# Kernel tuning notes

Measured on AMD Instinct MI355X. Metric: run time of the kernel, lower is better.

Reference implementation:

```python
import jax, jax.numpy as jnp
import numpy as np

N_NODES = 50000
N_EDGES = 800000
NODE_DIM = 32
EDGE_DIM = 16
HIDDEN = 64


def setup_inputs() -> dict:
    key = jax.random.key(0)
    ks = jax.random.split(key, 7)
    h = jax.random.normal(ks[0], (N_NODES, HIDDEN), dtype=jnp.float32)
    nf = jax.random.normal(ks[1], (N_NODES, NODE_DIM), dtype=jnp.float32)
    ef = jax.random.normal(ks[2], (N_EDGES, EDGE_DIM), dtype=jnp.float32)
    src = jax.random.randint(ks[3], (N_EDGES,), 0, N_NODES, dtype=jnp.int32)
    dst = jax.random.randint(ks[4], (N_EDGES,), 0, N_NODES, dtype=jnp.int32)
    # torch Linear weights: [out_features, in_features]
    in1 = HIDDEN + 2 * NODE_DIM + EDGE_DIM  # 144
    W1 = jax.random.normal(ks[5], (HIDDEN, in1), dtype=jnp.float32) * (1.0 / np.sqrt(in1))
    W2 = jax.random.normal(ks[6], (HIDDEN, HIDDEN), dtype=jnp.float32) * (1.0 / np.sqrt(HIDDEN))
    return {"h": h, "nf": nf, "ef": ef, "src": src, "dst": dst, "W1": W1, "W2": W2}


def reference(h, nf, ef, src, dst, W1, W2):
    n = nf.shape[0]
    # per-edge message: concat(dst.x, edge.x, src.h)  -> [E, node+edge+hidden]
    m_e = jnp.concatenate([nf[dst], ef, h[src]], axis=-1)
    # mailbox sum per destination node
    m = jax.ops.segment_sum(m_e, dst, num_segments=n)  # [N, node+edge+hidden]
    z = jnp.concatenate([nf, m], axis=-1)              # [N, hidden+2*node+edge]
    new_h = jax.nn.relu(z @ W1.T) @ W2.T               # [N, hidden]
    # DGL update_all only updates nodes that received at least one message
    deg = jax.ops.segment_sum(jnp.ones_like(dst, dtype=jnp.float32), dst, num_segments=n)
    return jnp.where(deg[:, None] > 0, new_h, h)
```

## Files before the change

### kernel.cpp

```cpp
#include <hip/hip_runtime.h>

#define NDIM 32
#define EDIM 16
#define NHID 64
#define NIN1 144
#define SCHUNK 1024
#define SPT 4

__global__ __launch_bounds__(256) void sse_hist(
    const int* __restrict__ dst, int* __restrict__ counts,
    int* __restrict__ rank,
    const float* __restrict__ W1, float* __restrict__ W1T,
    const float* __restrict__ W2, float* __restrict__ W2T, int E) {
  int e = blockIdx.x * 256 + threadIdx.x;
  if (e < NHID * NIN1) {
    int r = e / NIN1, k = e - r * NIN1;
    W1T[k * NHID + r] = W1[e];
  } else if (e < NHID * NIN1 + NHID * NHID) {
    int i = e - NHID * NIN1;
    int r = i >> 6, k = i & 63;
    W2T[k * NHID + r] = W2[i];
  }
  if (e < E) rank[e] = atomicAdd(&counts[dst[e]], 1);
}

__global__ __launch_bounds__(256) void sse_scan_part(
    const int* __restrict__ counts, int* __restrict__ bsum, int N) {
  __shared__ int ws[4];
  int t = threadIdx.x;
  int base = blockIdx.x * SCHUNK + t * SPT;
  int s = 0;
#pragma unroll
  for (int i = 0; i < SPT; ++i) {
    int idx = base + i;
    if (idx < N) s += counts[idx];
  }
  int v = s;
#pragma unroll
  for (int off = 1; off < 64; off <<= 1) v += __shfl_xor(v, off, 64);
  if ((t & 63) == 0) ws[t >> 6] = v;
  __syncthreads();
  if (t == 0) bsum[blockIdx.x] = ws[0] + ws[1] + ws[2] + ws[3];
}

__global__ __launch_bounds__(256) void sse_scan_final(
    const int* __restrict__ counts, const int* __restrict__ bsum,
    int* __restrict__ starts, int N, int nb) {
  __shared__ int ws[4];
  int t = threadIdx.x;
  int lane = t & 63, w = t >> 6;
  int boff = 0;
  for (int j = 0; j < (int)blockIdx.x; ++j) boff += bsum[j];
  int base = blockIdx.x * SCHUNK + t * SPT;
  int c[SPT];
  int s = 0;
#pragma unroll
  for (int i = 0; i < SPT; ++i) {
    int idx = base + i;
    c[i] = (idx < N) ? counts[idx] : 0;
    s += c[i];
  }
  int incl = s;
#pragma unroll
  for (int off = 1; off < 64; off <<= 1) {
    int u = __shfl_up(incl, off, 64);
    if (lane >= off) incl += u;
  }
  if (lane == 63) ws[w] = incl;
  __syncthreads();
  int woff = 0;
#pragma unroll
  for (int j = 0; j < 4; ++j)
    if (j < w) woff += ws[j];
  int run = boff + woff + (incl - s);
#pragma unroll
  for (int i = 0; i < SPT; ++i) {
    int idx = base + i;
    if (idx < N) {
      starts[idx] = run;
      run += c[i];
    }
  }
  if ((int)blockIdx.x == nb - 1 && t == 0)
    starts[N] = boff + ws[0] + ws[1] + ws[2] + ws[3];
}

__global__ __launch_bounds__(256) void sse_build(
    const int* __restrict__ src, const int* __restrict__ dst,
    const int* __restrict__ rank, const int* __restrict__ starts,
    int2* __restrict__ sedge, int E) {
  int e = blockIdx.x * 256 + threadIdx.x;
  if (e >= E) return;
  int d = dst[e];
  int pos = starts[d] + rank[e];
  sedge[pos] = make_int2(src[e], e);
}

__global__ __launch_bounds__(256) void sse_gather(
    const float* __restrict__ h, const float* __restrict__ ef,
    const int* __restrict__ starts, const int2* __restrict__ sedge,
    float* __restrict__ efsum, float* __restrict__ hsum, int N) {
  int node = blockIdx.x * 4 + (threadIdx.x >> 6);
  int lane = threadIdx.x & 63;
  if (node >= N) return;
  int st = starts[node], en = starts[node + 1];
  const float4* h4 = (const float4*)h;
  const float4* ef4 = (const float4*)ef;

  int q = lane >> 4, m = lane & 15;
  float4 ha = make_float4(0.f, 0.f, 0.f, 0.f);
  int j = st;
  for (; j + 7 < en; j += 8) {
    int s0 = sedge[j + q].x;
    int s1 = sedge[j + 4 + q].x;
    float4 v0 = h4[(size_t)s0 * 16 + m];
    float4 v1 = h4[(size_t)s1 * 16 + m];
    ha.x += v0.x + v1.x;
    ha.y += v0.y + v1.y;
    ha.z += v0.z + v1.z;
    ha.w += v0.w + v1.w;
  }
  if (j + 3 < en) {
    int s0 = sedge[j + q].x;
    float4 v0 = h4[(size_t)s0 * 16 + m];
    ha.x += v0.x; ha.y += v0.y; ha.z += v0.z; ha.w += v0.w;
    j += 4;
  }
  if (j + q < en) {
    int s0 = sedge[j + q].x;
    float4 v0 = h4[(size_t)s0 * 16 + m];
    ha.x += v0.x; ha.y += v0.y; ha.z += v0.z; ha.w += v0.w;
  }
#pragma unroll
  for (int off = 16; off < 64; off <<= 1) {
    ha.x += __shfl_xor(ha.x, off, 64);
    ha.y += __shfl_xor(ha.y, off, 64);
    ha.z += __shfl_xor(ha.z, off, 64);
    ha.w += __shfl_xor(ha.w, off, 64);
  }
  if (lane < 16) ((float4*)hsum)[(size_t)node * 16 + m] = ha;

  int eq = lane >> 2, em = lane & 3;
  float4 ea = make_float4(0.f, 0.f, 0.f, 0.f);
  for (j = st; j + 15 < en; j += 16) {
    int eid = sedge[j + eq].y;
    float4 v = ef4[(size_t)eid * 4 + em];
    ea.x += v.x; ea.y += v.y; ea.z += v.z; ea.w += v.w;
  }
  if (j + eq < en) {
    int eid = sedge[j + eq].y;
    float4 v = ef4[(size_t)eid * 4 + em];
    ea.x += v.x; ea.y += v.y; ea.z += v.z; ea.w += v.w;
  }
#pragma unroll
  for (int off = 4; off < 64; off <<= 1) {
    ea.x += __shfl_xor(ea.x, off, 64);
    ea.y += __shfl_xor(ea.y, off, 64);
    ea.z += __shfl_xor(ea.z, off, 64);
    ea.w += __shfl_xor(ea.w, off, 64);
  }
  if (lane < 4) ((float4*)efsum)[(size_t)node * 4 + em] = ea;
}

__global__ __launch_bounds__(256) void sse_node(
    const float* __restrict__ h, const float* __restrict__ nf,
    const float* __restrict__ efsum, const float* __restrict__ hsum,
    const int* __restrict__ starts, const float* __restrict__ W1T,
    const float* __restrict__ W2T, float* __restrict__ out, int N) {
  __shared__ float4 zs[36 * 64];
  __shared__ float4 as[16 * 64];

  int tid = threadIdx.x;
  int lane = tid & 63;
  int w = __builtin_amdgcn_readfirstlane(tid) >> 6;

  int node = blockIdx.x * 64 + lane;
  int nodeC = node < N ? node : N - 1;

  if (w == 0) {
    int st = starts[nodeC], en = starts[nodeC + 1];
    float dg = (float)(en - st);
    const float4* nfr = (const float4*)(nf + (size_t)nodeC * NDIM);
#pragma unroll
    for (int k4 = 0; k4 < 8; ++k4) {
      float4 v = nfr[k4];
      zs[k4 * 64 + lane] = v;
      zs[(8 + k4) * 64 + lane] =
          make_float4(dg * v.x, dg * v.y, dg * v.z, dg * v.w);
    }
  } else if (w == 1) {
    const float4* efr = (const float4*)(efsum + (size_t)nodeC * EDIM);
#pragma unroll
    for (int k4 = 0; k4 < 4; ++k4) zs[(16 + k4) * 64 + lane] = efr[k4];
  } else if (w == 2) {
    const float4* hsr = (const float4*)(hsum + (size_t)nodeC * NHID);
#pragma unroll
    for (int k4 = 0; k4 < 8; ++k4) zs[(20 + k4) * 64 + lane] = hsr[k4];
  } else {
    const float4* hsr = (const float4*)(hsum + (size_t)nodeC * NHID);
#pragma unroll
    for (int k4 = 8; k4 < 16; ++k4) zs[(20 + k4) * 64 + lane] = hsr[k4];
  }
  __syncthreads();

  const float4* w1b = (const float4*)W1T + w * 4;
  float a[16];
#pragma unroll
  for (int j = 0; j < 16; ++j) a[j] = 0.f;

#pragma unroll 2
  for (int k4 = 0; k4 < 36; ++k4) {
    float4 zv = zs[k4 * 64 + lane];
#pragma unroll
    for (int kk = 0; kk < 4; ++kk) {
      int k = k4 * 4 + kk;
      float4 w0 = w1b[k * 16 + 0];
      float4 w1 = w1b[k * 16 + 1];
      float4 w2 = w1b[k * 16 + 2];
      float4 w3 = w1b[k * 16 + 3];
      float zk = kk == 0 ? zv.x : kk == 1 ? zv.y : kk == 2 ? zv.z : zv.w;
      a[0]  = fmaf(w0.x, zk, a[0]);
      a[1]  = fmaf(w0.y, zk, a[1]);
      a[2]  = fmaf(w0.z, zk, a[2]);
      a[3]  = fmaf(w0.w, zk, a[3]);
      a[4]  = fmaf(w1.x, zk, a[4]);
      a[5]  = fmaf(w1.y, zk, a[5]);
      a[6]  = fmaf(w1.z, zk, a[6]);
      a[7]  = fmaf(w1.w, zk, a[7]);
      a[8]  = fmaf(w2.x, zk, a[8]);
      a[9]  = fmaf(w2.y, zk, a[9]);
      a[10] = fmaf(w2.z, zk, a[10]);
      a[11] = fmaf(w2.w, zk, a[11]);
      a[12] = fmaf(w3.x, zk, a[12]);
      a[13] = fmaf(w3.y, zk, a[13]);
      a[14] = fmaf(w3.z, zk, a[14]);
      a[15] = fmaf(w3.w, zk, a[15]);
    }
  }

#pragma unroll
  for (int j4 = 0; j4 < 4; ++j4)
    as[(w * 4 + j4) * 64 + lane] =
        make_float4(fmaxf(a[j4 * 4 + 0], 0.f), fmaxf(a[j4 * 4 + 1], 0.f),
                    fmaxf(a[j4 * 4 + 2], 0.f), fmaxf(a[j4 * 4 + 3], 0.f));
  __syncthreads();

  const float4* w2b = (const float4*)W2T + w * 4;
  float o[16];
#pragma unroll
  for (int j = 0; j < 16; ++j) o[j] = 0.f;

#pragma unroll 2
  for (int kq = 0; kq < 16; ++kq) {
    float4 av = as[kq * 64 + lane];
#pragma unroll
    for (int kk = 0; kk < 4; ++kk) {
      int k = kq * 4 + kk;
      float4 w0 = w2b[k * 16 + 0];
      float4 w1 = w2b[k * 16 + 1];
      float4 w2 = w2b[k * 16 + 2];
      float4 w3 = w2b[k * 16 + 3];
      float ak = kk == 0 ? av.x : kk == 1 ? av.y : kk == 2 ? av.z : av.w;
      o[0]  = fmaf(w0.x, ak, o[0]);
      o[1]  = fmaf(w0.y, ak, o[1]);
      o[2]  = fmaf(w0.z, ak, o[2]);
      o[3]  = fmaf(w0.w, ak, o[3]);
      o[4]  = fmaf(w1.x, ak, o[4]);
      o[5]  = fmaf(w1.y, ak, o[5]);
      o[6]  = fmaf(w1.z, ak, o[6]);
      o[7]  = fmaf(w1.w, ak, o[7]);
      o[8]  = fmaf(w2.x, ak, o[8]);
      o[9]  = fmaf(w2.y, ak, o[9]);
      o[10] = fmaf(w2.z, ak, o[10]);
      o[11] = fmaf(w2.w, ak, o[11]);
      o[12] = fmaf(w3.x, ak, o[12]);
      o[13] = fmaf(w3.y, ak, o[13]);
      o[14] = fmaf(w3.z, ak, o[14]);
      o[15] = fmaf(w3.w, ak, o[15]);
    }
  }

  if (node < N) {
    int st = starts[node], en = starts[node + 1];
    float4* o4 = (float4*)(out + (size_t)node * NHID + w * 16);
    if (en - st == 0) {
      const float4* hr = (const float4*)(h + (size_t)node * NHID + w * 16);
#pragma unroll
      for (int j4 = 0; j4 < 4; ++j4) o4[j4] = hr[j4];
    } else {
#pragma unroll
      for (int j4 = 0; j4 < 4; ++j4)
        o4[j4] = make_float4(o[j4 * 4 + 0], o[j4 * 4 + 1], o[j4 * 4 + 2],
                             o[j4 * 4 + 3]);
    }
  }
}

extern "C" void kernel_launch(void* const* d_in, const int* in_sizes, int n_in,
                              void* d_out, int out_size, void* d_ws, size_t ws_size,
                              hipStream_t stream) {
  const float* h  = (const float*)d_in[0];
  const float* nf = (const float*)d_in[1];
  const float* ef = (const float*)d_in[2];
  const int*   src = (const int*)d_in[3];
  const int*   dst = (const int*)d_in[4];
  const float* W1 = (const float*)d_in[5];
  const float* W2 = (const float*)d_in[6];
  float* out = (float*)d_out;

  int N = in_sizes[0] / NHID;
  int E = in_sizes[3];

  char* p = (char*)d_ws;
  int2* sedge = (int2*)p;                 p += (size_t)E * 8;
  int* counts = (int*)p;                  p += (size_t)N * 4;
  int* starts = (int*)p;                  p += (size_t)(N + 1) * 4;
  int* bsum = (int*)p;                    p += 64 * 4;
  float* W1T = (float*)p;                 p += (size_t)NIN1 * NHID * 4;
  float* W2T = (float*)p;                 p += (size_t)NHID * NHID * 4;
  p = (char*)(((size_t)p + 15) & ~(size_t)15);
  float* efsum = (float*)p;               p += (size_t)N * EDIM * 4;
  float* hsum = (float*)p;
  int* rank = (int*)hsum;

  hipMemsetAsync(counts, 0, (size_t)N * sizeof(int), stream);

  int eblocks = (E + 255) / 256;
  int nb = (N + SCHUNK - 1) / SCHUNK;

  sse_hist<<<eblocks, 256, 0, stream>>>(dst, counts, rank, W1, W1T, W2, W2T, E);
  sse_scan_part<<<nb, 256, 0, stream>>>(counts, bsum, N);
  sse_scan_final<<<nb, 256, 0, stream>>>(counts, bsum, starts, N, nb);
  sse_build<<<eblocks, 256, 0, stream>>>(src, dst, rank, starts, sedge, E);

  int gblocks = (N + 3) / 4;
  sse_gather<<<gblocks, 256, 0, stream>>>(h, ef, starts, sedge, efsum, hsum, N);

  int nblocks = (N + 63) / 64;
  sse_node<<<nblocks, 256, 0, stream>>>(h, nf, efsum, hsum, starts, W1T, W2T,
                                        out, N);
}
```

Baseline: 237.8 us.

## Process two nodes per wave in gather and batch four edges per thread

The gather kernel now gives each wave two destination nodes instead of one. It loads each node's sorted edge records once, coalesced, in chunks of 64 and hands source and edge ids to lanes with shuffles. It then issues eight h-row loads and two edge-feature loads per iteration, so more independent memory requests are in flight and the edge list is no longer read twice for the h and ef passes. The histogram and bucket-build kernels each handle four edges per thread with a quarter of the blocks, and the histogram issues its atomics before storing the ranks. The cost is more register pressure in gather, and imbalance when the two nodes in a wave have very different degrees.

```diff
diff --git a/kernel.cpp b/kernel.cpp
--- a/kernel.cpp
+++ b/kernel.cpp
@@ -12,16 +12,27 @@
     int* __restrict__ rank,
     const float* __restrict__ W1, float* __restrict__ W1T,
     const float* __restrict__ W2, float* __restrict__ W2T, int E) {
-  int e = blockIdx.x * 256 + threadIdx.x;
-  if (e < NHID * NIN1) {
-    int r = e / NIN1, k = e - r * NIN1;
-    W1T[k * NHID + r] = W1[e];
-  } else if (e < NHID * NIN1 + NHID * NHID) {
-    int i = e - NHID * NIN1;
+  int t = blockIdx.x * 256 + threadIdx.x;
+  if (t < NHID * NIN1) {
+    int r = t / NIN1, k = t - r * NIN1;
+    W1T[k * NHID + r] = W1[t];
+  } else if (t < NHID * NIN1 + NHID * NHID) {
+    int i = t - NHID * NIN1;
     int r = i >> 6, k = i & 63;
     W2T[k * NHID + r] = W2[i];
   }
-  if (e < E) rank[e] = atomicAdd(&counts[dst[e]], 1);
+  int ebase = blockIdx.x * 1024 + threadIdx.x;
+  int r[4];
+#pragma unroll
+  for (int i = 0; i < 4; ++i) {
+    int e = ebase + i * 256;
+    if (e < E) r[i] = atomicAdd(&counts[dst[e]], 1);
+  }
+#pragma unroll
+  for (int i = 0; i < 4; ++i) {
+    int e = ebase + i * 256;
+    if (e < E) rank[e] = r[i];
+  }
 }
 
 __global__ __launch_bounds__(256) void sse_scan_part(
@@ -89,77 +100,121 @@
     const int* __restrict__ src, const int* __restrict__ dst,
     const int* __restrict__ rank, const int* __restrict__ starts,
     int2* __restrict__ sedge, int E) {
-  int e = blockIdx.x * 256 + threadIdx.x;
-  if (e >= E) return;
-  int d = dst[e];
-  int pos = starts[d] + rank[e];
-  sedge[pos] = make_int2(src[e], e);
+  int ebase = blockIdx.x * 1024 + threadIdx.x;
+#pragma unroll
+  for (int i = 0; i < 4; ++i) {
+    int e = ebase + i * 256;
+    if (e < E) {
+      int d = dst[e];
+      int pos = starts[d] + rank[e];
+      sedge[pos] = make_int2(src[e], e);
+    }
+  }
 }
 
 __global__ __launch_bounds__(256) void sse_gather(
     const float* __restrict__ h, const float* __restrict__ ef,
     const int* __restrict__ starts, const int2* __restrict__ sedge,
     float* __restrict__ efsum, float* __restrict__ hsum, int N) {
-  int node = blockIdx.x * 4 + (threadIdx.x >> 6);
+  int w = threadIdx.x >> 6;
   int lane = threadIdx.x & 63;
-  if (node >= N) return;
-  int st = starts[node], en = starts[node + 1];
+  int nodeA = blockIdx.x * 8 + w * 2;
+  if (nodeA >= N) return;
+  int nodeB = nodeA + 1;
+  bool vB = nodeB < N;
+
+  int stA = starts[nodeA], enA = starts[nodeA + 1];
+  int stB = 0, enB = 0;
+  if (vB) { stB = starts[nodeB]; enB = starts[nodeB + 1]; }
+
   const float4* h4 = (const float4*)h;
   const float4* ef4 = (const float4*)ef;
-
   int q = lane >> 4, m = lane & 15;
-  float4 ha = make_float4(0.f, 0.f, 0.f, 0.f);
-  int j = st;
-  for (; j + 7 < en; j += 8) {
-    int s0 = sedge[j + q].x;
-    int s1 = sedge[j + 4 + q].x;
-    float4 v0 = h4[(size_t)s0 * 16 + m];
-    float4 v1 = h4[(size_t)s1 * 16 + m];
-    ha.x += v0.x + v1.x;
-    ha.y += v0.y + v1.y;
-    ha.z += v0.z + v1.z;
-    ha.w += v0.w + v1.w;
-  }
-  if (j + 3 < en) {
-    int s0 = sedge[j + q].x;
-    float4 v0 = h4[(size_t)s0 * 16 + m];
-    ha.x += v0.x; ha.y += v0.y; ha.z += v0.z; ha.w += v0.w;
-    j += 4;
-  }
-  if (j + q < en) {
-    int s0 = sedge[j + q].x;
-    float4 v0 = h4[(size_t)s0 * 16 + m];
-    ha.x += v0.x; ha.y += v0.y; ha.z += v0.z; ha.w += v0.w;
-  }
+  int eq = lane >> 2, em = lane & 3;
+
+  float4 haA = make_float4(0.f, 0.f, 0.f, 0.f);
+  float4 haB = make_float4(0.f, 0.f, 0.f, 0.f);
+  float4 eaA = make_float4(0.f, 0.f, 0.f, 0.f);
+  float4 eaB = make_float4(0.f, 0.f, 0.f, 0.f);
+
+  int baseA = stA, baseB = stB;
+  while (baseA < enA || baseB < enB) {
+    int CA = enA - baseA; CA = CA < 0 ? 0 : (CA > 64 ? 64 : CA);
+    int CB = enB - baseB; CB = CB < 0 ? 0 : (CB > 64 ? 64 : CB);
+    int2 segA = (lane < CA) ? sedge[baseA + lane] : make_int2(0, 0);
+    int2 segB = (lane < CB) ? sedge[baseB + lane] : make_int2(0, 0);
+    int mySA = segA.x, myEA = segA.y;
+    int mySB = segB.x, myEB = segB.y;
+    int rA = (CA + 15) >> 4, rB = (CB + 15) >> 4;
+    int rM = rA > rB ? rA : rB;
+    for (int r = 0; r < rM; ++r) {
+      int ba = (r < rA) ? r * 16 : 64;
+      int bb = (r < rB) ? r * 16 : 64;
+      int a0 = ba + q, a1 = ba + 4 + q, a2 = ba + 8 + q, a3 = ba + 12 + q;
+      int b0 = bb + q, b1 = bb + 4 + q, b2 = bb + 8 + q, b3 = bb + 12 + q;
+      int ae = ba + eq, be = bb + eq;
+      int s0 = __shfl(mySA, a0 & 63, 64);
+      int s1 = __shfl(mySA, a1 & 63, 64);
+      int s2 = __shfl(mySA, a2 & 63, 64);
+      int s3 = __shfl(mySA, a3 & 63, 64);
+      int t0 = __shfl(mySB, b0 & 63, 64);
+      int t1 = __shfl(mySB, b1 & 63, 64);
+      int t2 = __shfl(mySB, b2 & 63, 64);
+      int t3 = __shfl(mySB, b3 & 63, 64);
+      int eidA = __shfl(myEA, ae & 63, 64);
+      int eidB = __shfl(myEB, be & 63, 64);
+      float4 va0 = h4[(size_t)s0 * 16 + m];
+      float4 va1 = h4[(size_t)s1 * 16 + m];
+      float4 va2 = h4[(size_t)s2 * 16 + m];
+      float4 va3 = h4[(size_t)s3 * 16 + m];
+      float4 vb0 = h4[(size_t)t0 * 16 + m];
+      float4 vb1 = h4[(size_t)t1 * 16 + m];
+      float4 vb2 = h4[(size_t)t2 * 16 + m];
+      float4 vb3 = h4[(size_t)t3 * 16 + m];
+      float4 evA = ef4[(size_t)eidA * 4 + em];
+      float4 evB = ef4[(size_t)eidB * 4 + em];
+      if (a0 < CA) { haA.x += va0.x; haA.y += va0.y; haA.z += va0.z; haA.w += va0.w; }
+      if (a1 < CA) { haA.x += va1.x; haA.y += va1.y; haA.z += va1.z; haA.w += va1.w; }
+      if (a2 < CA) { haA.x += va2.x; haA.y += va2.y; haA.z += va2.z; haA.w += va2.w; }
+      if (a3 < CA) { haA.x += va3.x; haA.y += va3.y; haA.z += va3.z; haA.w += va3.w; }
+      if (b0 < CB) { haB.x += vb0.x; haB.y += vb0.y; haB.z += vb0.z; haB.w += vb0.w; }
+      if (b1 < CB) { haB.x += vb1.x; haB.y += vb1.y; haB.z += vb1.z; haB.w += vb1.w; }
+      if (b2 < CB) { haB.x += vb2.x; haB.y += vb2.y; haB.z += vb2.z; haB.w += vb2.w; }
+      if (b3 < CB) { haB.x += vb3.x; haB.y += vb3.y; haB.z += vb3.z; haB.w += vb3.w; }
+      if (ae < CA) { eaA.x += evA.x; eaA.y += evA.y; eaA.z += evA.z; eaA.w += evA.w; }
+      if (be < CB) { eaB.x += evB.x; eaB.y += evB.y; eaB.z += evB.z; eaB.w += evB.w; }
+    }
+    baseA += 64;
+    baseB += 64;
+  }
+
 #pragma unroll
   for (int off = 16; off < 64; off <<= 1) {
-    ha.x += __shfl_xor(ha.x, off, 64);
-    ha.y += __shfl_xor(ha.y, off, 64);
-    ha.z += __shfl_xor(ha.z, off, 64);
-    ha.w += __shfl_xor(ha.w, off, 64);
-  }
-  if (lane < 16) ((float4*)hsum)[(size_t)node * 16 + m] = ha;
-
-  int eq = lane >> 2, em = lane & 3;
-  float4 ea = make_float4(0.f, 0.f, 0.f, 0.f);
-  for (j = st; j + 15 < en; j += 16) {
-    int eid = sedge[j + eq].y;
-    float4 v = ef4[(size_t)eid * 4 + em];
-    ea.x += v.x; ea.y += v.y; ea.z += v.z; ea.w += v.w;
-  }
-  if (j + eq < en) {
-    int eid = sedge[j + eq].y;
-    float4 v = ef4[(size_t)eid * 4 + em];
-    ea.x += v.x; ea.y += v.y; ea.z += v.z; ea.w += v.w;
-  }
+    haA.x += __shfl_xor(haA.x, off, 64);
+    haA.y += __shfl_xor(haA.y, off, 64);
+    haA.z += __shfl_xor(haA.z, off, 64);
+    haA.w += __shfl_xor(haA.w, off, 64);
+    haB.x += __shfl_xor(haB.x, off, 64);
+    haB.y += __shfl_xor(haB.y, off, 64);
+    haB.z += __shfl_xor(haB.z, off, 64);
+    haB.w += __shfl_xor(haB.w, off, 64);
+  }
+  if (lane < 16) ((float4*)hsum)[(size_t)nodeA * 16 + m] = haA;
+  if (vB && lane < 16) ((float4*)hsum)[(size_t)nodeB * 16 + m] = haB;
+
 #pragma unroll
   for (int off = 4; off < 64; off <<= 1) {
-    ea.x += __shfl_xor(ea.x, off, 64);
-    ea.y += __shfl_xor(ea.y, off, 64);
-    ea.z += __shfl_xor(ea.z, off, 64);
-    ea.w += __shfl_xor(ea.w, off, 64);
-  }
-  if (lane < 4) ((float4*)efsum)[(size_t)node * 4 + em] = ea;
+    eaA.x += __shfl_xor(eaA.x, off, 64);
+    eaA.y += __shfl_xor(eaA.y, off, 64);
+    eaA.z += __shfl_xor(eaA.z, off, 64);
+    eaA.w += __shfl_xor(eaA.w, off, 64);
+    eaB.x += __shfl_xor(eaB.x, off, 64);
+    eaB.y += __shfl_xor(eaB.y, off, 64);
+    eaB.z += __shfl_xor(eaB.z, off, 64);
+    eaB.w += __shfl_xor(eaB.w, off, 64);
+  }
+  if (lane < 4) ((float4*)efsum)[(size_t)nodeA * 4 + em] = eaA;
+  if (vB && lane < 4) ((float4*)efsum)[(size_t)nodeB * 4 + em] = eaB;
 }
 
 __global__ __launch_bounds__(256) void sse_node(
@@ -325,15 +380,15 @@
 
   hipMemsetAsync(counts, 0, (size_t)N * sizeof(int), stream);
 
-  int eblocks = (E + 255) / 256;
+  int eblocks4 = (E + 1023) / 1024;
   int nb = (N + SCHUNK - 1) / SCHUNK;
 
-  sse_hist<<<eblocks, 256, 0, stream>>>(dst, counts, rank, W1, W1T, W2, W2T, E);
+  sse_hist<<<eblocks4, 256, 0, stream>>>(dst, counts, rank, W1, W1T, W2, W2T, E);
   sse_scan_part<<<nb, 256, 0, stream>>>(counts, bsum, N);
   sse_scan_final<<<nb, 256, 0, stream>>>(counts, bsum, starts, N, nb);
-  sse_build<<<eblocks, 256, 0, stream>>>(src, dst, rank, starts, sedge, E);
-
-  int gblocks = (N + 3) / 4;
+  sse_build<<<eblocks4, 256, 0, stream>>>(src, dst, rank, starts, sedge, E);
+
+  int gblocks = (N + 7) / 8;
   sse_gather<<<gblocks, 256, 0, stream>>>(h, ef, starts, sedge, efsum, hsum, N);
 
   int nblocks = (N + 63) / 64;
```

After: 232.9 us. 1.02x faster.

## Convert h and edge features to bf16 before gather, store sums in bf16

Applied to the files above, without the earlier changes.

The histogram kernel now also converts h (and ef, when workspace allows) to packed bf16, so the random-access gather reads half the bytes per neighbor row. The gather loads sedge once per 64-edge chunk and broadcasts indices with shuffles, handling four h rows per pass with 8 lanes each. Per-node sums are written in bf16 and unpacked in the node MLP kernel. The hist and build kernels each process four edges per thread. The cost is a full extra pass to convert ef (800k×16 floats), which may offset the gather savings, plus bf16 rounding error in the inputs and the sums.

```diff
diff --git a/kernel.cpp b/kernel.cpp
--- a/kernel.cpp
+++ b/kernel.cpp
@@ -7,21 +7,78 @@
 #define SCHUNK 1024
 #define SPT 4
 
+__device__ __forceinline__ unsigned pk2(float a, float b) {
+  unsigned ua = __float_as_uint(a);
+  unsigned ub = __float_as_uint(b);
+  ua = (ua + 0x7FFFu + ((ua >> 16) & 1u)) >> 16;
+  ub = (ub + 0x7FFFu + ((ub >> 16) & 1u)) >> 16;
+  return ua | (ub << 16);
+}
+__device__ __forceinline__ float lo16(unsigned u) { return __uint_as_float(u << 16); }
+__device__ __forceinline__ float hi16(unsigned u) { return __uint_as_float(u & 0xFFFF0000u); }
+
+#define ACC8(A, V)                                   \
+  do {                                               \
+    A[0] += lo16((V).x); A[1] += hi16((V).x);        \
+    A[2] += lo16((V).y); A[3] += hi16((V).y);        \
+    A[4] += lo16((V).z); A[5] += hi16((V).z);        \
+    A[6] += lo16((V).w); A[7] += hi16((V).w);        \
+  } while (0)
+
 __global__ __launch_bounds__(256) void sse_hist(
     const int* __restrict__ dst, int* __restrict__ counts,
     int* __restrict__ rank,
     const float* __restrict__ W1, float* __restrict__ W1T,
-    const float* __restrict__ W2, float* __restrict__ W2T, int E) {
-  int e = blockIdx.x * 256 + threadIdx.x;
-  if (e < NHID * NIN1) {
-    int r = e / NIN1, k = e - r * NIN1;
-    W1T[k * NHID + r] = W1[e];
-  } else if (e < NHID * NIN1 + NHID * NHID) {
-    int i = e - NHID * NIN1;
-    int r = i >> 6, k = i & 63;
-    W2T[k * NHID + r] = W2[i];
-  }
-  if (e < E) rank[e] = atomicAdd(&counts[dst[e]], 1);
+    const float* __restrict__ W2, float* __restrict__ W2T,
+    const float* __restrict__ h, uint4* __restrict__ h16,
+    const float* __restrict__ ef, uint4* __restrict__ ef16,
+    int E, int N) {
+  int t = blockIdx.x * 256 + threadIdx.x;
+  int T = gridDim.x * 256;
+
+  int ebase = blockIdx.x * 1024 + threadIdx.x;
+  int r[4];
+#pragma unroll
+  for (int i = 0; i < 4; ++i) {
+    int e = ebase + i * 256;
+    if (e < E) r[i] = atomicAdd(&counts[dst[e]], 1);
+  }
+
+  if (t < NHID * NIN1) {
+    int rr = t / NIN1, k = t - rr * NIN1;
+    W1T[k * NHID + rr] = W1[t];
+  } else if (t < NHID * NIN1 + NHID * NHID) {
+    int i = t - NHID * NIN1;
+    int rr = i >> 6, k = i & 63;
+    W2T[k * NHID + rr] = W2[i];
+  }
+
+  const float4* hf4 = (const float4*)h;
+  int NH = N * 8;
+  for (int i = t; i < NH; i += T) {
+    float4 x = hf4[2 * i], y = hf4[2 * i + 1];
+    uint4 o;
+    o.x = pk2(x.x, x.y); o.y = pk2(x.z, x.w);
+    o.z = pk2(y.x, y.y); o.w = pk2(y.z, y.w);
+    h16[i] = o;
+  }
+  if (ef16) {
+    const float4* ef4 = (const float4*)ef;
+    int NE = E * 2;
+    for (int i = t; i < NE; i += T) {
+      float4 x = ef4[2 * i], y = ef4[2 * i + 1];
+      uint4 o;
+      o.x = pk2(x.x, x.y); o.y = pk2(x.z, x.w);
+      o.z = pk2(y.x, y.y); o.w = pk2(y.z, y.w);
+      ef16[i] = o;
+    }
+  }
+
+#pragma unroll
+  for (int i = 0; i < 4; ++i) {
+    int e = ebase + i * 256;
+    if (e < E) rank[e] = r[i];
+  }
 }
 
 __global__ __launch_bounds__(256) void sse_scan_part(
@@ -89,82 +146,153 @@
     const int* __restrict__ src, const int* __restrict__ dst,
     const int* __restrict__ rank, const int* __restrict__ starts,
     int2* __restrict__ sedge, int E) {
-  int e = blockIdx.x * 256 + threadIdx.x;
-  if (e >= E) return;
-  int d = dst[e];
-  int pos = starts[d] + rank[e];
-  sedge[pos] = make_int2(src[e], e);
+  int ebase = blockIdx.x * 1024 + threadIdx.x;
+#pragma unroll
+  for (int i = 0; i < 4; ++i) {
+    int e = ebase + i * 256;
+    if (e < E) {
+      int d = dst[e];
+      int pos = starts[d] + rank[e];
+      sedge[pos] = make_int2(src[e], e);
+    }
+  }
 }
 
 __global__ __launch_bounds__(256) void sse_gather(
-    const float* __restrict__ h, const float* __restrict__ ef,
+    const uint4* __restrict__ h16, const float* __restrict__ ef,
+    const uint4* __restrict__ ef16,
     const int* __restrict__ starts, const int2* __restrict__ sedge,
-    float* __restrict__ efsum, float* __restrict__ hsum, int N) {
-  int node = blockIdx.x * 4 + (threadIdx.x >> 6);
+    uint4* __restrict__ efsum16, uint4* __restrict__ hsum16, int N) {
+  int w = threadIdx.x >> 6;
   int lane = threadIdx.x & 63;
+  int node = blockIdx.x * 4 + w;
   if (node >= N) return;
   int st = starts[node], en = starts[node + 1];
-  const float4* h4 = (const float4*)h;
-  const float4* ef4 = (const float4*)ef;
-
-  int q = lane >> 4, m = lane & 15;
-  float4 ha = make_float4(0.f, 0.f, 0.f, 0.f);
-  int j = st;
-  for (; j + 7 < en; j += 8) {
-    int s0 = sedge[j + q].x;
-    int s1 = sedge[j + 4 + q].x;
-    float4 v0 = h4[(size_t)s0 * 16 + m];
-    float4 v1 = h4[(size_t)s1 * 16 + m];
-    ha.x += v0.x + v1.x;
-    ha.y += v0.y + v1.y;
-    ha.z += v0.z + v1.z;
-    ha.w += v0.w + v1.w;
-  }
-  if (j + 3 < en) {
-    int s0 = sedge[j + q].x;
-    float4 v0 = h4[(size_t)s0 * 16 + m];
-    ha.x += v0.x; ha.y += v0.y; ha.z += v0.z; ha.w += v0.w;
-    j += 4;
-  }
-  if (j + q < en) {
-    int s0 = sedge[j + q].x;
-    float4 v0 = h4[(size_t)s0 * 16 + m];
-    ha.x += v0.x; ha.y += v0.y; ha.z += v0.z; ha.w += v0.w;
-  }
-#pragma unroll
-  for (int off = 16; off < 64; off <<= 1) {
-    ha.x += __shfl_xor(ha.x, off, 64);
-    ha.y += __shfl_xor(ha.y, off, 64);
-    ha.z += __shfl_xor(ha.z, off, 64);
-    ha.w += __shfl_xor(ha.w, off, 64);
-  }
-  if (lane < 16) ((float4*)hsum)[(size_t)node * 16 + m] = ha;
-
-  int eq = lane >> 2, em = lane & 3;
-  float4 ea = make_float4(0.f, 0.f, 0.f, 0.f);
-  for (j = st; j + 15 < en; j += 16) {
-    int eid = sedge[j + eq].y;
-    float4 v = ef4[(size_t)eid * 4 + em];
-    ea.x += v.x; ea.y += v.y; ea.z += v.z; ea.w += v.w;
-  }
-  if (j + eq < en) {
-    int eid = sedge[j + eq].y;
-    float4 v = ef4[(size_t)eid * 4 + em];
-    ea.x += v.x; ea.y += v.y; ea.z += v.z; ea.w += v.w;
-  }
-#pragma unroll
-  for (int off = 4; off < 64; off <<= 1) {
-    ea.x += __shfl_xor(ea.x, off, 64);
-    ea.y += __shfl_xor(ea.y, off, 64);
-    ea.z += __shfl_xor(ea.z, off, 64);
-    ea.w += __shfl_xor(ea.w, off, 64);
-  }
-  if (lane < 4) ((float4*)efsum)[(size_t)node * 4 + em] = ea;
+
+  int q8 = lane >> 3, m = lane & 7;
+  float acc[8];
+#pragma unroll
+  for (int i = 0; i < 8; ++i) acc[i] = 0.f;
+
+  if (ef16) {
+    int eq2 = lane >> 1, em2 = lane & 1;
+    float ea8[8];
+#pragma unroll
+    for (int i = 0; i < 8; ++i) ea8[i] = 0.f;
+
+    for (int base = st; base < en; base += 64) {
+      int C = en - base; C = C > 64 ? 64 : C;
+      int2 seg = (lane < C) ? sedge[base + lane] : make_int2(0, 0);
+      int myS = seg.x, myE = seg.y;
+      int nr = (C + 31) >> 5;
+      for (int r = 0; r < nr; ++r) {
+        int b = r * 32;
+        int i0 = b + q8, i1 = b + 8 + q8, i2 = b + 16 + q8, i3 = b + 24 + q8;
+        int s0 = __shfl(myS, i0, 64);
+        int s1 = __shfl(myS, i1, 64);
+        int s2 = __shfl(myS, i2, 64);
+        int s3 = __shfl(myS, i3, 64);
+        int ie = b + eq2;
+        int eid = __shfl(myE, ie, 64);
+        uint4 v0 = h16[(size_t)s0 * 8 + m];
+        uint4 v1 = h16[(size_t)s1 * 8 + m];
+        uint4 v2 = h16[(size_t)s2 * 8 + m];
+        uint4 v3 = h16[(size_t)s3 * 8 + m];
+        uint4 ev = ef16[(size_t)eid * 2 + em2];
+        if (i0 < C) ACC8(acc, v0);
+        if (i1 < C) ACC8(acc, v1);
+        if (i2 < C) ACC8(acc, v2);
+        if (i3 < C) ACC8(acc, v3);
+        if (ie < C) ACC8(ea8, ev);
+      }
+    }
+#pragma unroll
+    for (int off = 8; off < 64; off <<= 1)
+#pragma unroll
+      for (int i = 0; i < 8; ++i) acc[i] += __shfl_xor(acc[i], off, 64);
+    if (lane < 8) {
+      uint4 o;
+      o.x = pk2(acc[0], acc[1]); o.y = pk2(acc[2], acc[3]);
+      o.z = pk2(acc[4], acc[5]); o.w = pk2(acc[6], acc[7]);
+      hsum16[(size_t)node * 8 + lane] = o;
+    }
+#pragma unroll
+    for (int off = 2; off < 64; off <<= 1)
+#pragma unroll
+      for (int i = 0; i < 8; ++i) ea8[i] += __shfl_xor(ea8[i], off, 64);
+    if (lane < 2) {
+      uint4 o;
+      o.x = pk2(ea8[0], ea8[1]); o.y = pk2(ea8[2], ea8[3]);
+      o.z = pk2(ea8[4], ea8[5]); o.w = pk2(ea8[6], ea8[7]);
+      efsum16[(size_t)node * 2 + lane] = o;
+    }
+  } else {
+    int eq = lane >> 2, em = lane & 3;
+    const float4* ef4 = (const float4*)ef;
+    float4 ea = make_float4(0.f, 0.f, 0.f, 0.f);
+
+    for (int base = st; base < en; base += 64) {
+      int C = en - base; C = C > 64 ? 64 : C;
+      int2 seg = (lane < C) ? sedge[base + lane] : make_int2(0, 0);
+      int myS = seg.x, myE = seg.y;
+      int nr = (C + 31) >> 5;
+      for (int r = 0; r < nr; ++r) {
+        int b = r * 32;
+        int i0 = b + q8, i1 = b + 8 + q8, i2 = b + 16 + q8, i3 = b + 24 + q8;
+        int s0 = __shfl(myS, i0, 64);
+        int s1 = __shfl(myS, i1, 64);
+        int s2 = __shfl(myS, i2, 64);
+        int s3 = __shfl(myS, i3, 64);
+        int e0 = b + eq, e1 = b + 16 + eq;
+        int id0 = __shfl(myE, e0, 64);
+        int id1 = __shfl(myE, e1, 64);
+        uint4 v0 = h16[(size_t)s0 * 8 + m];
+        uint4 v1 = h16[(size_t)s1 * 8 + m];
+        uint4 v2 = h16[(size_t)s2 * 8 + m];
+        uint4 v3 = h16[(size_t)s3 * 8 + m];
+        float4 x0 = ef4[(size_t)id0 * 4 + em];
+        float4 x1 = ef4[(size_t)id1 * 4 + em];
+        if (i0 < C) ACC8(acc, v0);
+        if (i1 < C) ACC8(acc, v1);
+        if (i2 < C) ACC8(acc, v2);
+        if (i3 < C) ACC8(acc, v3);
+        if (e0 < C) { ea.x += x0.x; ea.y += x0.y; ea.z += x0.z; ea.w += x0.w; }
+        if (e1 < C) { ea.x += x1.x; ea.y += x1.y; ea.z += x1.z; ea.w += x1.w; }
+      }
+    }
+#pragma unroll
+    for (int off = 8; off < 64; off <<= 1)
+#pragma unroll
+      for (int i = 0; i < 8; ++i) acc[i] += __shfl_xor(acc[i], off, 64);
+    if (lane < 8) {
+      uint4 o;
+      o.x = pk2(acc[0], acc[1]); o.y = pk2(acc[2], acc[3]);
+      o.z = pk2(acc[4], acc[5]); o.w = pk2(acc[6], acc[7]);
+      hsum16[(size_t)node * 8 + lane] = o;
+    }
+#pragma unroll
+    for (int off = 4; off < 64; off <<= 1) {
+      ea.x += __shfl_xor(ea.x, off, 64);
+      ea.y += __shfl_xor(ea.y, off, 64);
+      ea.z += __shfl_xor(ea.z, off, 64);
+      ea.w += __shfl_xor(ea.w, off, 64);
+    }
+    float bx = __shfl_xor(ea.x, 1, 64);
+    float by = __shfl_xor(ea.y, 1, 64);
+    float bz = __shfl_xor(ea.z, 1, 64);
+    float bw = __shfl_xor(ea.w, 1, 64);
+    if (lane < 4 && (lane & 1) == 0) {
+      uint4 o;
+      o.x = pk2(ea.x, ea.y); o.y = pk2(ea.z, ea.w);
+      o.z = pk2(bx, by);     o.w = pk2(bz, bw);
+      efsum16[(size_t)node * 2 + (lane >> 1)] = o;
+    }
+  }
 }
 
 __global__ __launch_bounds__(256) void sse_node(
     const float* __restrict__ h, const float* __restrict__ nf,
-    const float* __restrict__ efsum, const float* __restrict__ hsum,
+    const uint4* __restrict__ efsum16, const uint4* __restrict__ hsum16,
     const int* __restrict__ starts, const float* __restrict__ W1T,
     const float* __restrict__ W2T, float* __restrict__ out, int N) {
   __shared__ float4 zs[36 * 64];
@@ -189,17 +317,30 @@
           make_float4(dg * v.x, dg * v.y, dg * v.z, dg * v.w);
     }
   } else if (w == 1) {
-    const float4* efr = (const float4*)(efsum + (size_t)nodeC * EDIM);
-#pragma unroll
-    for (int k4 = 0; k4 < 4; ++k4) zs[(16 + k4) * 64 + lane] = efr[k4];
+    uint4 a = efsum16[(size_t)nodeC * 2 + 0];
+    uint4 b = efsum16[(size_t)nodeC * 2 + 1];
+    zs[16 * 64 + lane] = make_float4(lo16(a.x), hi16(a.x), lo16(a.y), hi16(a.y));
+    zs[17 * 64 + lane] = make_float4(lo16(a.z), hi16(a.z), lo16(a.w), hi16(a.w));
+    zs[18 * 64 + lane] = make_float4(lo16(b.x), hi16(b.x), lo16(b.y), hi16(b.y));
+    zs[19 * 64 + lane] = make_float4(lo16(b.z), hi16(b.z), lo16(b.w), hi16(b.w));
   } else if (w == 2) {
-    const float4* hsr = (const float4*)(hsum + (size_t)nodeC * NHID);
-#pragma unroll
-    for (int k4 = 0; k4 < 8; ++k4) zs[(20 + k4) * 64 + lane] = hsr[k4];
+#pragma unroll
+    for (int c = 0; c < 4; ++c) {
+      uint4 u = hsum16[(size_t)nodeC * 8 + c];
+      zs[(20 + 2 * c) * 64 + lane] =
+          make_float4(lo16(u.x), hi16(u.x), lo16(u.y), hi16(u.y));
+      zs[(21 + 2 * c) * 64 + lane] =
+          make_float4(lo16(u.z), hi16(u.z), lo16(u.w), hi16(u.w));
+    }
   } else {
-    const float4* hsr = (const float4*)(hsum + (size_t)nodeC * NHID);
-#pragma unroll
-    for (int k4 = 8; k4 < 16; ++k4) zs[(20 + k4) * 64 + lane] = hsr[k4];
+#pragma unroll
+    for (int c = 4; c < 8; ++c) {
+      uint4 u = hsum16[(size_t)nodeC * 8 + c];
+      zs[(20 + 2 * c) * 64 + lane] =
+          make_float4(lo16(u.x), hi16(u.x), lo16(u.y), hi16(u.y));
+      zs[(21 + 2 * c) * 64 + lane] =
+          make_float4(lo16(u.z), hi16(u.z), lo16(u.w), hi16(u.w));
+    }
   }
   __syncthreads();
 
@@ -319,24 +460,30 @@
   float* W1T = (float*)p;                 p += (size_t)NIN1 * NHID * 4;
   float* W2T = (float*)p;                 p += (size_t)NHID * NHID * 4;
   p = (char*)(((size_t)p + 15) & ~(size_t)15);
-  float* efsum = (float*)p;               p += (size_t)N * EDIM * 4;
-  float* hsum = (float*)p;
-  int* rank = (int*)hsum;
+  uint4* h16 = (uint4*)p;                 p += (size_t)N * 128;
+  uint4* efsum16 = (uint4*)p;             p += (size_t)N * 32;
+  uint4* hsum16 = (uint4*)p;              p += (size_t)N * 128;
+  int* rank = (int*)hsum16;
+  uint4* ef16 = (uint4*)p;
+  size_t base_used = (size_t)((char*)p - (char*)d_ws);
+  if (base_used + (size_t)E * 32 > ws_size) ef16 = nullptr;
 
   hipMemsetAsync(counts, 0, (size_t)N * sizeof(int), stream);
 
-  int eblocks = (E + 255) / 256;
+  int eblocks4 = (E + 1023) / 1024;
   int nb = (N + SCHUNK - 1) / SCHUNK;
 
-  sse_hist<<<eblocks, 256, 0, stream>>>(dst, counts, rank, W1, W1T, W2, W2T, E);
+  sse_hist<<<eblocks4, 256, 0, stream>>>(dst, counts, rank, W1, W1T, W2, W2T,
+                                         h, h16, ef, ef16, E, N);
   sse_scan_part<<<nb, 256, 0, stream>>>(counts, bsum, N);
   sse_scan_final<<<nb, 256, 0, stream>>>(counts, bsum, starts, N, nb);
-  sse_build<<<eblocks, 256, 0, stream>>>(src, dst, rank, starts, sedge, E);
+  sse_build<<<eblocks4, 256, 0, stream>>>(src, dst, rank, starts, sedge, E);
 
   int gblocks = (N + 3) / 4;
-  sse_gather<<<gblocks, 256, 0, stream>>>(h, ef, starts, sedge, efsum, hsum, N);
+  sse_gather<<<gblocks, 256, 0, stream>>>(h16, ef, ef16, starts, sedge,
+                                          efsum16, hsum16, N);
 
   int nblocks = (N + 63) / 64;
-  sse_node<<<nblocks, 256, 0, stream>>>(h, nf, efsum, hsum, starts, W1T, W2T,
-                                        out, N);
-}
+  sse_node<<<nblocks, 256, 0, stream>>>(h, nf, efsum16, hsum16, starts, W1T,
+                                        W2T, out, N);
+}
```

New measurement: 255.2 us. 7.3% more time.
